# Optimization experiments

Hardware: AMD Instinct MI355X
Metric: run time of the kernel (lower is better)

## Reference

```python
import jax, jax.numpy as jnp
import numpy as np

BS, N, C_IMG, C_PT, H, W = 8, 100000, 512, 256, 48, 160


def setup_inputs() -> dict:
    key = jax.random.key(0)
    ks = jax.random.split(key, 8)
    point_feat = jax.random.normal(ks[0], (N, C_PT), dtype=jnp.float32)
    # pillar centers in LiDAR frame: x forward [10,60], y left [-10,10], z [-2,1]
    u = jax.random.uniform(ks[1], (N, 3), dtype=jnp.float32)
    pillar_centers = jnp.stack([
        10.0 + 50.0 * u[:, 0],
        -10.0 + 20.0 * u[:, 1],
        -2.0 + 3.0 * u[:, 2],
    ], axis=1)
    batch_idx = jax.random.randint(ks[2], (N,), 0, BS, dtype=jnp.int32)
    img_feat = jax.random.normal(ks[3], (BS, C_IMG, H, W), dtype=jnp.float32)
    # KITTI-style calibration (per batch, small jitter)
    f, cx, cy = 80.0, 80.0, 24.0
    P2_base = np.array([[f, 0, cx, 0], [0, f, cy, 0], [0, 0, 1, 0]], dtype=np.float32)
    Tr_base = np.array([[0, -1, 0, 0], [0, 0, -1, 0], [1, 0, 0, 0], [0, 0, 0, 1]], dtype=np.float32)
    rng = np.random.RandomState(0)
    P2 = np.stack([P2_base + 0.01 * rng.randn(3, 4).astype(np.float32) for _ in range(BS)])
    R0 = np.stack([np.eye(4, dtype=np.float32) for _ in range(BS)])
    Tr = np.stack([Tr_base + 0.001 * rng.randn(4, 4).astype(np.float32) for _ in range(BS)])
    align_w = jax.random.normal(ks[4], (C_PT, C_IMG), dtype=jnp.float32) * 0.02
    align_b = jax.random.normal(ks[5], (C_PT,), dtype=jnp.float32) * 0.02
    return {
        'point_feat': point_feat, 'pillar_centers': pillar_centers,
        'img_feat': img_feat, 'P2': jnp.asarray(P2), 'R0': jnp.asarray(R0),
        'Tr': jnp.asarray(Tr), 'align_w': align_w, 'align_b': align_b,
        'batch_idx': batch_idx, 'img_h': H, 'img_w': W,
    }


def _fuse(point_feat, pillar_centers, img_feat, P2, R0, Tr, align_w, align_b,
          batch_idx, img_h, img_w):
    n = point_feat.shape[0]
    dt = point_feat.dtype
    # --- project_to_image (vectorized over all points via per-point calib gather) ---
    pts_hom = jnp.concatenate([pillar_centers, jnp.ones((n, 1), dtype=dt)], axis=1)  # [N,4]
    pts_cam = jnp.einsum('nij,nj->ni', Tr[batch_idx], pts_hom)    # [N,4]
    pts_rect = jnp.einsum('nij,nj->ni', R0[batch_idx], pts_cam)   # [N,4]
    pts_img = jnp.einsum('nij,nj->ni', P2[batch_idx], pts_rect)   # [N,3]
    depth = jnp.clip(pts_img[:, 2:3], 1e-5, None)
    uv = pts_img[:, :2] / depth
    valid = ((pts_img[:, 2] > 0) & (uv[:, 0] >= 0) & (uv[:, 0] < img_w)
             & (uv[:, 1] >= 0) & (uv[:, 1] < img_h))
    # --- grid_sample bilinear, align_corners=True, padding_mode='zeros' ---
    # grid = 2*uv/(dim-1)-1 with align_corners=True => pixel coords == uv.
    _, C, Hf, Wf = img_feat.shape
    u_, v_ = uv[:, 0], uv[:, 1]
    x0 = jnp.floor(u_); y0 = jnp.floor(v_)
    wx1 = u_ - x0; wx0 = 1.0 - wx1
    wy1 = v_ - y0; wy0 = 1.0 - wy1

    def gather(xi, yi):
        inb = (xi >= 0) & (xi <= Wf - 1) & (yi >= 0) & (yi <= Hf - 1)
        xc = jnp.clip(xi, 0, Wf - 1).astype(jnp.int32)
        yc = jnp.clip(yi, 0, Hf - 1).astype(jnp.int32)
        f = img_feat[batch_idx, :, yc, xc]  # [N,C]
        return f * inb.astype(dt)[:, None]

    sampled = (gather(x0, y0) * (wx0 * wy0)[:, None]
               + gather(x0 + 1, y0) * (wx1 * wy0)[:, None]
               + gather(x0, y0 + 1) * (wx0 * wy1)[:, None]
               + gather(x0 + 1, y0 + 1) * (wx1 * wy1)[:, None])
    sampled = jnp.where(valid[:, None], sampled, jnp.zeros((), dtype=dt))
    # --- align (Linear) + residual add ---
    aligned = sampled @ align_w.T + align_b
    return point_feat + aligned


def reference(point_feat, pillar_centers, img_feat, P2, R0, Tr, align_w, align_b,
              batch_idx, img_h, img_w):
    return _fuse(point_feat, pillar_centers, img_feat, P2, R0, Tr,
                 align_w, align_b, batch_idx, img_h, img_w)
```

## Files before the change

### kernel.cpp

```cpp
#include <hip/hip_runtime.h>

#define C_IMG 512
#define C_PT  256
#define IMG_H 48
#define IMG_W 160
#define HWPIX (IMG_H * IMG_W)

#define MP   64
#define BK   64
#define SPAD 72

typedef short bf16x8 __attribute__((ext_vector_type(8)));
typedef float f32x4  __attribute__((ext_vector_type(4)));

static __device__ __forceinline__ unsigned short f2bf(float f) {
    unsigned u = __float_as_uint(f);
    u += 0x7fffu + ((u >> 16) & 1u);
    return (unsigned short)(u >> 16);
}
static __device__ __forceinline__ unsigned pack2(float lo, float hi) {
    return (unsigned)f2bf(lo) | ((unsigned)f2bf(hi) << 16);
}
static __device__ __forceinline__ float bflo(unsigned v) { return __uint_as_float(v << 16); }
static __device__ __forceinline__ float bfhi(unsigned v) { return __uint_as_float(v & 0xffff0000u); }

__global__ __launch_bounds__(256)
void cvt_w_kernel(const float* __restrict__ alw, unsigned short* __restrict__ alwT) {
    const int i = (blockIdx.x * 256 + threadIdx.x) * 8;
    const float4 a = *(const float4*)(alw + i);
    const float4 b = *(const float4*)(alw + i + 4);
    uint4 o;
    o.x = pack2(a.x, a.y); o.y = pack2(a.z, a.w);
    o.z = pack2(b.x, b.y); o.w = pack2(b.z, b.w);
    *(uint4*)(alwT + i) = o;
}

__global__ __launch_bounds__(256)
void proj_kernel(const float* __restrict__ img,
                 const unsigned short* __restrict__ wbf,
                 unsigned short* __restrict__ PT) {
    const int blk  = blockIdx.x;
    const int b    = blk / (HWPIX / 64);
    const int hw0  = (blk % (HWPIX / 64)) * 64;
    const int tid  = threadIdx.x;
    const int lane = tid & 63;
    const int wid  = tid >> 6;
    const int l15  = lane & 15;
    const int quad = lane >> 4;

    f32x4 acc[4][4];
    #pragma unroll
    for (int i = 0; i < 4; ++i)
        #pragma unroll
        for (int j = 0; j < 4; ++j)
            acc[i][j] = (f32x4){0.f, 0.f, 0.f, 0.f};

    const float* aim = img + (size_t)b * C_IMG * HWPIX + hw0 + l15;
    const unsigned short* bw = wbf + (size_t)(wid * 64 + l15) * C_IMG + quad * 8;

    for (int ck = 0; ck < C_IMG / 64; ++ck) {
        #pragma unroll
        for (int kk = 0; kk < 2; ++kk) {
            const int c0 = ck * 64 + kk * 32 + quad * 8;
            bf16x8 af[4];
            #pragma unroll
            for (int mt = 0; mt < 4; ++mt) {
                const float* ap = aim + (size_t)c0 * HWPIX + mt * 16;
                float f[8];
                #pragma unroll
                for (int j = 0; j < 8; ++j) f[j] = ap[j * HWPIX];
                union { unsigned u[4]; bf16x8 v; } cv;
                cv.u[0] = pack2(f[0], f[1]);
                cv.u[1] = pack2(f[2], f[3]);
                cv.u[2] = pack2(f[4], f[5]);
                cv.u[3] = pack2(f[6], f[7]);
                af[mt] = cv.v;
            }
            bf16x8 bfr[4];
            #pragma unroll
            for (int nt = 0; nt < 4; ++nt)
                bfr[nt] = *(const bf16x8*)(bw + (size_t)(nt * 16) * C_IMG + ck * 64 + kk * 32);
            #pragma unroll
            for (int mt = 0; mt < 4; ++mt)
                #pragma unroll
                for (int nt = 0; nt < 4; ++nt)
                    acc[mt][nt] = __builtin_amdgcn_mfma_f32_16x16x32_bf16(
                        af[mt], bfr[nt], acc[mt][nt], 0, 0, 0);
        }
    }

    #pragma unroll
    for (int mt = 0; mt < 4; ++mt) {
        #pragma unroll
        for (int r = 0; r < 4; ++r) {
            const int pix = mt * 16 + quad * 4 + r;
            unsigned short* dst = PT + (size_t)(b * HWPIX + hw0 + pix) * C_PT;
            #pragma unroll
            for (int nt = 0; nt < 4; ++nt) {
                const int nc = wid * 64 + nt * 16 + l15;
                dst[nc] = f2bf(acc[mt][nt][r]);
            }
        }
    }
}

#define PPW 4
__global__ __launch_bounds__(256)
void point_kernel(const float* __restrict__ pf,
                  const float* __restrict__ centers,
                  const unsigned short* __restrict__ PT,
                  const float* __restrict__ P2,
                  const float* __restrict__ R0,
                  const float* __restrict__ Tr,
                  const float* __restrict__ alb,
                  const int*   __restrict__ bidx,
                  float* __restrict__ out,
                  int n)
{
    const int tid  = threadIdx.x;
    const int lane = tid & 63;
    const int wid  = tid >> 6;
    const int p0   = blockIdx.x * (4 * PPW) + wid * PPW;

    const float4 ab = *(const float4*)(alb + lane * 4);

    #pragma unroll
    for (int it = 0; it < PPW; ++it) {
        const int p = p0 + it;
        if (p >= n) break;

        const float cx = centers[p * 3 + 0];
        const float cy = centers[p * 3 + 1];
        const float cz = centers[p * 3 + 2];
        const int   b  = bidx[p];
        const float* tr = Tr + b * 16;
        const float c0 = tr[0]*cx + tr[1]*cy + tr[2]*cz + tr[3];
        const float c1 = tr[4]*cx + tr[5]*cy + tr[6]*cz + tr[7];
        const float c2 = tr[8]*cx + tr[9]*cy + tr[10]*cz + tr[11];
        const float c3 = tr[12]*cx + tr[13]*cy + tr[14]*cz + tr[15];
        const float* r0 = R0 + b * 16;
        const float e0 = r0[0]*c0 + r0[1]*c1 + r0[2]*c2 + r0[3]*c3;
        const float e1 = r0[4]*c0 + r0[5]*c1 + r0[6]*c2 + r0[7]*c3;
        const float e2 = r0[8]*c0 + r0[9]*c1 + r0[10]*c2 + r0[11]*c3;
        const float e3 = r0[12]*c0 + r0[13]*c1 + r0[14]*c2 + r0[15]*c3;
        const float* p2 = P2 + b * 12;
        const float ix = p2[0]*e0 + p2[1]*e1 + p2[2]*e2  + p2[3]*e3;
        const float iy = p2[4]*e0 + p2[5]*e1 + p2[6]*e2  + p2[7]*e3;
        const float iz = p2[8]*e0 + p2[9]*e1 + p2[10]*e2 + p2[11]*e3;
        const float depth = fmaxf(iz, 1e-5f);
        const float u = ix / depth;
        const float v = iy / depth;
        const bool valid = (iz > 0.f) && (u >= 0.f) && (u < (float)IMG_W)
                                     && (v >= 0.f) && (v < (float)IMG_H);
        const float x0f = floorf(u), y0f = floorf(v);
        const float wx1 = u - x0f, wx0 = 1.f - wx1;
        const float wy1 = v - y0f, wy0 = 1.f - wy1;
        const float cwv[4] = {wx0 * wy0, wx1 * wy0, wx0 * wy1, wx1 * wy1};
        float wgt[4]; int off[4];
        #pragma unroll
        for (int j = 0; j < 4; ++j) {
            const float xf = x0f + (float)(j & 1);
            const float yf = y0f + (float)(j >> 1);
            const bool inb = (xf >= 0.f) && (xf <= (float)(IMG_W - 1))
                          && (yf >= 0.f) && (yf <= (float)(IMG_H - 1));
            const int xc = (int)fminf(fmaxf(xf, 0.f), (float)(IMG_W - 1));
            const int yc = (int)fminf(fmaxf(yf, 0.f), (float)(IMG_H - 1));
            wgt[j] = (valid && inb) ? cwv[j] : 0.f;
            off[j] = ((b * IMG_H + yc) * IMG_W + xc) * C_PT;
        }

        float s0 = 0.f, s1 = 0.f, s2 = 0.f, s3 = 0.f;
        #pragma unroll
        for (int j = 0; j < 4; ++j) {
            const uint2 g = *(const uint2*)(PT + off[j] + lane * 4);
            s0 = fmaf(wgt[j], bflo(g.x), s0);
            s1 = fmaf(wgt[j], bfhi(g.x), s1);
            s2 = fmaf(wgt[j], bflo(g.y), s2);
            s3 = fmaf(wgt[j], bfhi(g.y), s3);
        }

        const size_t idx = (size_t)p * C_PT + lane * 4;
        const float4 pv = *(const float4*)(pf + idx);
        float4 ov;
        ov.x = pv.x + ab.x + s0;
        ov.y = pv.y + ab.y + s1;
        ov.z = pv.z + ab.z + s2;
        ov.w = pv.w + ab.w + s3;
        *(float4*)(out + idx) = ov;
    }
}

__global__ __launch_bounds__(256)
void fused_fallback_kernel(const float* __restrict__ pf,
                           const float* __restrict__ centers,
                           const float* __restrict__ img,
                           const float* __restrict__ P2,
                           const float* __restrict__ R0,
                           const float* __restrict__ Tr,
                           const float* __restrict__ alw,
                           const float* __restrict__ alb,
                           const int*   __restrict__ bidx,
                           float* __restrict__ out,
                           int n)
{
    __shared__ float          sWg[MP][4];
    __shared__ int            sOf[MP][4];
    __shared__ unsigned short sS[MP][SPAD];
    __shared__ unsigned short sW[C_PT][SPAD];

    const int tid = threadIdx.x;
    const int pt0 = blockIdx.x * MP;

    if (tid < MP) {
        const int p = pt0 + tid;
        float w[4] = {0.f, 0.f, 0.f, 0.f};
        int   o[4] = {0, 0, 0, 0};
        if (p < n) {
            const float cx = centers[p * 3 + 0];
            const float cy = centers[p * 3 + 1];
            const float cz = centers[p * 3 + 2];
            const int   b  = bidx[p];
            const float* tr = Tr + b * 16;
            const float c0 = tr[0]*cx + tr[1]*cy + tr[2]*cz + tr[3];
            const float c1 = tr[4]*cx + tr[5]*cy + tr[6]*cz + tr[7];
            const float c2 = tr[8]*cx + tr[9]*cy + tr[10]*cz + tr[11];
            const float c3 = tr[12]*cx + tr[13]*cy + tr[14]*cz + tr[15];
            const float* r0 = R0 + b * 16;
            const float e0 = r0[0]*c0 + r0[1]*c1 + r0[2]*c2 + r0[3]*c3;
            const float e1 = r0[4]*c0 + r0[5]*c1 + r0[6]*c2 + r0[7]*c3;
            const float e2 = r0[8]*c0 + r0[9]*c1 + r0[10]*c2 + r0[11]*c3;
            const float e3 = r0[12]*c0 + r0[13]*c1 + r0[14]*c2 + r0[15]*c3;
            const float* p2 = P2 + b * 12;
            const float ix = p2[0]*e0 + p2[1]*e1 + p2[2]*e2  + p2[3]*e3;
            const float iy = p2[4]*e0 + p2[5]*e1 + p2[6]*e2  + p2[7]*e3;
            const float iz = p2[8]*e0 + p2[9]*e1 + p2[10]*e2 + p2[11]*e3;
            const float depth = fmaxf(iz, 1e-5f);
            const float u = ix / depth;
            const float v = iy / depth;
            const bool valid = (iz > 0.f) && (u >= 0.f) && (u < (float)IMG_W)
                                         && (v >= 0.f) && (v < (float)IMG_H);
            const float x0f = floorf(u), y0f = floorf(v);
            const float wx1 = u - x0f, wx0 = 1.f - wx1;
            const float wy1 = v - y0f, wy0 = 1.f - wy1;
            const float cwv[4] = {wx0 * wy0, wx1 * wy0, wx0 * wy1, wx1 * wy1};
            #pragma unroll
            for (int j = 0; j < 4; ++j) {
                const float xf = x0f + (float)(j & 1);
                const float yf = y0f + (float)(j >> 1);
                const bool inb = (xf >= 0.f) && (xf <= (float)(IMG_W - 1))
                              && (yf >= 0.f) && (yf <= (float)(IMG_H - 1));
                const int xc = (int)fminf(fmaxf(xf, 0.f), (float)(IMG_W - 1));
                const int yc = (int)fminf(fmaxf(yf, 0.f), (float)(IMG_H - 1));
                w[j] = (valid && inb) ? cwv[j] : 0.f;
                o[j] = b * C_IMG * HWPIX + yc * IMG_W + xc;
            }
        }
        #pragma unroll
        for (int j = 0; j < 4; ++j) { sWg[tid][j] = w[j]; sOf[tid][j] = o[j]; }
    }

    f32x4 acc[4][4];
    #pragma unroll
    for (int i = 0; i < 4; ++i)
        #pragma unroll
        for (int j = 0; j < 4; ++j)
            acc[i][j] = (f32x4){0.f, 0.f, 0.f, 0.f};

    const int lane = tid & 63;
    const int wid  = tid >> 6;
    const int l15  = lane & 15;
    const int quad = lane >> 4;
    const int sp   = tid >> 2;
    const int ssub = tid & 3;

    __syncthreads();

    for (int ck = 0; ck < C_IMG / BK; ++ck) {
        {
            const float cw0 = sWg[sp][0], cw1 = sWg[sp][1], cw2 = sWg[sp][2], cw3 = sWg[sp][3];
            const int   co0 = sOf[sp][0], co1 = sOf[sp][1], co2 = sOf[sp][2], co3 = sOf[sp][3];
            const int   cb  = ck * BK + ssub * 16;
            const float* ib = img;
            #pragma unroll
            for (int h = 0; h < 2; ++h) {
                uint4 ov;
                unsigned* op = (unsigned*)&ov;
                #pragma unroll
                for (int wI = 0; wI < 4; ++wI) {
                    const int c = cb + h * 8 + 2 * wI;
                    const float vlo = cw0*ib[co0 + c*HWPIX] + cw1*ib[co1 + c*HWPIX]
                                    + cw2*ib[co2 + c*HWPIX] + cw3*ib[co3 + c*HWPIX];
                    const float vhi = cw0*ib[co0 + (c+1)*HWPIX] + cw1*ib[co1 + (c+1)*HWPIX]
                                    + cw2*ib[co2 + (c+1)*HWPIX] + cw3*ib[co3 + (c+1)*HWPIX];
                    op[wI] = pack2(vlo, vhi);
                }
                *(uint4*)&sS[sp][ssub * 16 + h * 8] = ov;
            }
        }
        {
            #pragma unroll
            for (int pass = 0; pass < 4; ++pass) {
                const int r = pass * 64 + (tid >> 2);
                const int c = (tid & 3) * 16;
                const float* wr = alw + (size_t)r * C_IMG + ck * BK + c;
                const float4 f0 = *(const float4*)(wr + 0);
                const float4 f1 = *(const float4*)(wr + 4);
                const float4 f2 = *(const float4*)(wr + 8);
                const float4 f3 = *(const float4*)(wr + 12);
                uint4 oa, ob;
                oa.x = pack2(f0.x, f0.y); oa.y = pack2(f0.z, f0.w);
                oa.z = pack2(f1.x, f1.y); oa.w = pack2(f1.z, f1.w);
                ob.x = pack2(f2.x, f2.y); ob.y = pack2(f2.z, f2.w);
                ob.z = pack2(f3.x, f3.y); ob.w = pack2(f3.z, f3.w);
                *(uint4*)&sW[r][c]     = oa;
                *(uint4*)&sW[r][c + 8] = ob;
            }
        }
        __syncthreads();

        #pragma unroll
        for (int kk = 0; kk < 2; ++kk) {
            bf16x8 af[4], bfr[4];
            #pragma unroll
            for (int mt = 0; mt < 4; ++mt)
                af[mt] = *(const bf16x8*)&sS[mt * 16 + l15][kk * 32 + quad * 8];
            #pragma unroll
            for (int nt = 0; nt < 4; ++nt)
                bfr[nt] = *(const bf16x8*)&sW[wid * 64 + nt * 16 + l15][kk * 32 + quad * 8];
            #pragma unroll
            for (int mt = 0; mt < 4; ++mt)
                #pragma unroll
                for (int nt = 0; nt < 4; ++nt)
                    acc[mt][nt] = __builtin_amdgcn_mfma_f32_16x16x32_bf16(
                        af[mt], bfr[nt], acc[mt][nt], 0, 0, 0);
        }
        __syncthreads();
    }

    #pragma unroll
    for (int mt = 0; mt < 4; ++mt) {
        #pragma unroll
        for (int r = 0; r < 4; ++r) {
            const int p = pt0 + mt * 16 + quad * 4 + r;
            if (p < n) {
                #pragma unroll
                for (int nt = 0; nt < 4; ++nt) {
                    const int nc = wid * 64 + nt * 16 + l15;
                    const size_t idx = (size_t)p * C_PT + nc;
                    out[idx] = pf[idx] + alb[nc] + acc[mt][nt][r];
                }
            }
        }
    }
}

extern "C" void kernel_launch(void* const* d_in, const int* in_sizes, int n_in,
                              void* d_out, int out_size, void* d_ws, size_t ws_size,
                              hipStream_t stream) {
    const float* pf      = (const float*)d_in[0];
    const float* centers = (const float*)d_in[1];
    const float* img     = (const float*)d_in[2];
    const float* P2      = (const float*)d_in[3];
    const float* R0      = (const float*)d_in[4];
    const float* Tr      = (const float*)d_in[5];
    const float* alw     = (const float*)d_in[6];
    const float* alb     = (const float*)d_in[7];
    const int*   bidx    = (const int*)d_in[8];
    float*       out     = (float*)d_out;

    const int n  = in_sizes[8];
    const int bs = in_sizes[3] / 12;

    const size_t tpt = (size_t)bs * HWPIX * C_PT * sizeof(unsigned short);
    const size_t tw  = (size_t)C_PT * C_IMG * sizeof(unsigned short);
    if (ws_size >= tpt + tw) {
        unsigned short* PT  = (unsigned short*)d_ws;
        unsigned short* wbf = (unsigned short*)((char*)d_ws + tpt);
        cvt_w_kernel<<<(C_PT * C_IMG / 8) / 256, 256, 0, stream>>>(alw, wbf);
        proj_kernel<<<bs * (HWPIX / 64), 256, 0, stream>>>(img, wbf, PT);
        point_kernel<<<(n + 4 * PPW * 4 - 1) / (4 * PPW * 4) * 4, 256, 0, stream>>>(
            pf, centers, PT, P2, R0, Tr, alb, bidx, out, n);
    } else {
        const int nblk = (n + MP - 1) / MP;
        fused_fallback_kernel<<<nblk, 256, 0, stream>>>(
            pf, centers, img, P2, R0, Tr, alw, alb, bidx, out, n);
    }
}
```

Before: 386.5 us.

## Stage image tiles in LDS, precompute point params, widen point gathers

The projection GEMM now loads the fp32 image channels through a double-buffered, swizzled LDS tile with coalesced float4 loads, replacing strided scalar global loads. It also uses cheaper round-half-up bf16 conversion. A new params kernel computes each point's bilinear offsets and weights once, and the point kernel reads them and gathers 8 channels per lane with nontemporal loads and stores on the dense point features. The cost is an extra kernel launch, extra workspace traffic, and slightly different bf16 rounding.

```diff
diff --git a/kernel.cpp b/kernel.cpp
--- a/kernel.cpp
+++ b/kernel.cpp
@@ -12,6 +12,7 @@
 
 typedef short bf16x8 __attribute__((ext_vector_type(8)));
 typedef float f32x4  __attribute__((ext_vector_type(4)));
+typedef unsigned u32x4 __attribute__((ext_vector_type(4)));
 
 static __device__ __forceinline__ unsigned short f2bf(float f) {
     unsigned u = __float_as_uint(f);
@@ -20,6 +21,13 @@
 }
 static __device__ __forceinline__ unsigned pack2(float lo, float hi) {
     return (unsigned)f2bf(lo) | ((unsigned)f2bf(hi) << 16);
+}
+static __device__ __forceinline__ unsigned short f2bf_hu(float f) {
+    return (unsigned short)((__float_as_uint(f) + 0x8000u) >> 16);
+}
+static __device__ __forceinline__ unsigned pack2_hu(float lo, float hi) {
+    return ((__float_as_uint(lo) + 0x8000u) >> 16)
+         | ((__float_as_uint(hi) + 0x8000u) & 0xffff0000u);
 }
 static __device__ __forceinline__ float bflo(unsigned v) { return __uint_as_float(v << 16); }
 static __device__ __forceinline__ float bfhi(unsigned v) { return __uint_as_float(v & 0xffff0000u); }
@@ -36,9 +44,66 @@
 }
 
 __global__ __launch_bounds__(256)
+void params_kernel(const float* __restrict__ centers,
+                   const float* __restrict__ P2,
+                   const float* __restrict__ R0,
+                   const float* __restrict__ Tr,
+                   const int*   __restrict__ bidx,
+                   u32x4* __restrict__ poff,
+                   f32x4* __restrict__ pwgt,
+                   int n)
+{
+    const int p = blockIdx.x * 256 + threadIdx.x;
+    if (p >= n) return;
+    const float cx = centers[p * 3 + 0];
+    const float cy = centers[p * 3 + 1];
+    const float cz = centers[p * 3 + 2];
+    const int   b  = bidx[p];
+    const float* tr = Tr + b * 16;
+    const float c0 = tr[0]*cx + tr[1]*cy + tr[2]*cz + tr[3];
+    const float c1 = tr[4]*cx + tr[5]*cy + tr[6]*cz + tr[7];
+    const float c2 = tr[8]*cx + tr[9]*cy + tr[10]*cz + tr[11];
+    const float c3 = tr[12]*cx + tr[13]*cy + tr[14]*cz + tr[15];
+    const float* r0 = R0 + b * 16;
+    const float e0 = r0[0]*c0 + r0[1]*c1 + r0[2]*c2 + r0[3]*c3;
+    const float e1 = r0[4]*c0 + r0[5]*c1 + r0[6]*c2 + r0[7]*c3;
+    const float e2 = r0[8]*c0 + r0[9]*c1 + r0[10]*c2 + r0[11]*c3;
+    const float e3 = r0[12]*c0 + r0[13]*c1 + r0[14]*c2 + r0[15]*c3;
+    const float* p2 = P2 + b * 12;
+    const float ix = p2[0]*e0 + p2[1]*e1 + p2[2]*e2  + p2[3]*e3;
+    const float iy = p2[4]*e0 + p2[5]*e1 + p2[6]*e2  + p2[7]*e3;
+    const float iz = p2[8]*e0 + p2[9]*e1 + p2[10]*e2 + p2[11]*e3;
+    const float depth = fmaxf(iz, 1e-5f);
+    const float u = ix / depth;
+    const float v = iy / depth;
+    const bool valid = (iz > 0.f) && (u >= 0.f) && (u < (float)IMG_W)
+                                 && (v >= 0.f) && (v < (float)IMG_H);
+    const float x0f = floorf(u), y0f = floorf(v);
+    const float wx1 = u - x0f, wx0 = 1.f - wx1;
+    const float wy1 = v - y0f, wy0 = 1.f - wy1;
+    const float cwv[4] = {wx0 * wy0, wx1 * wy0, wx0 * wy1, wx1 * wy1};
+    f32x4 wg; u32x4 of;
+    #pragma unroll
+    for (int j = 0; j < 4; ++j) {
+        const float xf = x0f + (float)(j & 1);
+        const float yf = y0f + (float)(j >> 1);
+        const bool inb = (xf >= 0.f) && (xf <= (float)(IMG_W - 1))
+                      && (yf >= 0.f) && (yf <= (float)(IMG_H - 1));
+        const int xc = (int)fminf(fmaxf(xf, 0.f), (float)(IMG_W - 1));
+        const int yc = (int)fminf(fmaxf(yf, 0.f), (float)(IMG_H - 1));
+        wg[j] = (valid && inb) ? cwv[j] : 0.f;
+        of[j] = (unsigned)(((b * IMG_H + yc) * IMG_W + xc) * C_PT);
+    }
+    poff[p] = of;
+    pwgt[p] = wg;
+}
+
+__global__ __launch_bounds__(256)
 void proj_kernel(const float* __restrict__ img,
                  const unsigned short* __restrict__ wbf,
-                 unsigned short* __restrict__ PT) {
+                 unsigned short* __restrict__ PT)
+{
+    __shared__ float sF[2][64][68];
     const int blk  = blockIdx.x;
     const int b    = blk / (HWPIX / 64);
     const int hw0  = (blk % (HWPIX / 64)) * 64;
@@ -48,6 +113,11 @@
     const int l15  = lane & 15;
     const int quad = lane >> 4;
 
+    const int sr   = tid >> 2;
+    const int scc  = tid & 3;
+    const int sdst = ((scc ^ ((sr >> 3) & 3)) << 4);
+    const float* gsrc = img + (size_t)b * C_IMG * HWPIX + hw0 + scc * 16;
+
     f32x4 acc[4][4];
     #pragma unroll
     for (int i = 0; i < 4; ++i)
@@ -55,31 +125,44 @@
         for (int j = 0; j < 4; ++j)
             acc[i][j] = (f32x4){0.f, 0.f, 0.f, 0.f};
 
-    const float* aim = img + (size_t)b * C_IMG * HWPIX + hw0 + l15;
     const unsigned short* bw = wbf + (size_t)(wid * 64 + l15) * C_IMG + quad * 8;
 
+    float4 st[4];
+    {
+        const float* gp = gsrc + (size_t)sr * HWPIX;
+        #pragma unroll
+        for (int k = 0; k < 4; ++k) st[k] = *(const float4*)(gp + 4 * k);
+        #pragma unroll
+        for (int k = 0; k < 4; ++k) *(float4*)&sF[0][sr][sdst + 4 * k] = st[k];
+    }
+    __syncthreads();
+
     for (int ck = 0; ck < C_IMG / 64; ++ck) {
+        const int cur = ck & 1;
+        if (ck < C_IMG / 64 - 1) {
+            const float* gp = gsrc + (size_t)((ck + 1) * 64 + sr) * HWPIX;
+            #pragma unroll
+            for (int k = 0; k < 4; ++k) st[k] = *(const float4*)(gp + 4 * k);
+        }
         #pragma unroll
         for (int kk = 0; kk < 2; ++kk) {
-            const int c0 = ck * 64 + kk * 32 + quad * 8;
-            bf16x8 af[4];
-            #pragma unroll
-            for (int mt = 0; mt < 4; ++mt) {
-                const float* ap = aim + (size_t)c0 * HWPIX + mt * 16;
-                float f[8];
-                #pragma unroll
-                for (int j = 0; j < 8; ++j) f[j] = ap[j * HWPIX];
-                union { unsigned u[4]; bf16x8 v; } cv;
-                cv.u[0] = pack2(f[0], f[1]);
-                cv.u[1] = pack2(f[2], f[3]);
-                cv.u[2] = pack2(f[4], f[5]);
-                cv.u[3] = pack2(f[6], f[7]);
-                af[mt] = cv.v;
-            }
-            bf16x8 bfr[4];
+            bf16x8 af[4], bfr[4];
             #pragma unroll
             for (int nt = 0; nt < 4; ++nt)
                 bfr[nt] = *(const bf16x8*)(bw + (size_t)(nt * 16) * C_IMG + ck * 64 + kk * 32);
+            const int rbase = kk * 32 + quad * 8;
+            #pragma unroll
+            for (int mt = 0; mt < 4; ++mt) {
+                const int col = ((mt ^ quad) << 4) + l15;
+                float f[8];
+                #pragma unroll
+                for (int j = 0; j < 8; ++j) f[j] = sF[cur][rbase + j][col];
+                union { unsigned u[4]; bf16x8 v; } cv;
+                #pragma unroll
+                for (int w2 = 0; w2 < 4; ++w2)
+                    cv.u[w2] = pack2_hu(f[2 * w2], f[2 * w2 + 1]);
+                af[mt] = cv.v;
+            }
             #pragma unroll
             for (int mt = 0; mt < 4; ++mt)
                 #pragma unroll
@@ -87,6 +170,11 @@
                     acc[mt][nt] = __builtin_amdgcn_mfma_f32_16x16x32_bf16(
                         af[mt], bfr[nt], acc[mt][nt], 0, 0, 0);
         }
+        if (ck < C_IMG / 64 - 1) {
+            #pragma unroll
+            for (int k = 0; k < 4; ++k) *(float4*)&sF[cur ^ 1][sr][sdst + 4 * k] = st[k];
+        }
+        __syncthreads();
     }
 
     #pragma unroll
@@ -94,99 +182,61 @@
         #pragma unroll
         for (int r = 0; r < 4; ++r) {
             const int pix = mt * 16 + quad * 4 + r;
-            unsigned short* dst = PT + (size_t)(b * HWPIX + hw0 + pix) * C_PT;
-            #pragma unroll
-            for (int nt = 0; nt < 4; ++nt) {
-                const int nc = wid * 64 + nt * 16 + l15;
-                dst[nc] = f2bf(acc[mt][nt][r]);
-            }
-        }
-    }
-}
-
-#define PPW 4
+            unsigned short* dst = PT + (size_t)(b * HWPIX + hw0 + pix) * C_PT + wid * 64 + l15;
+            #pragma unroll
+            for (int nt = 0; nt < 4; ++nt)
+                dst[nt * 16] = f2bf_hu(acc[mt][nt][r]);
+        }
+    }
+}
+
 __global__ __launch_bounds__(256)
 void point_kernel(const float* __restrict__ pf,
-                  const float* __restrict__ centers,
                   const unsigned short* __restrict__ PT,
-                  const float* __restrict__ P2,
-                  const float* __restrict__ R0,
-                  const float* __restrict__ Tr,
                   const float* __restrict__ alb,
-                  const int*   __restrict__ bidx,
+                  const u32x4* __restrict__ poff,
+                  const f32x4* __restrict__ pwgt,
                   float* __restrict__ out,
                   int n)
 {
     const int tid  = threadIdx.x;
     const int lane = tid & 63;
     const int wid  = tid >> 6;
-    const int p0   = blockIdx.x * (4 * PPW) + wid * PPW;
-
-    const float4 ab = *(const float4*)(alb + lane * 4);
-
-    #pragma unroll
-    for (int it = 0; it < PPW; ++it) {
-        const int p = p0 + it;
-        if (p >= n) break;
-
-        const float cx = centers[p * 3 + 0];
-        const float cy = centers[p * 3 + 1];
-        const float cz = centers[p * 3 + 2];
-        const int   b  = bidx[p];
-        const float* tr = Tr + b * 16;
-        const float c0 = tr[0]*cx + tr[1]*cy + tr[2]*cz + tr[3];
-        const float c1 = tr[4]*cx + tr[5]*cy + tr[6]*cz + tr[7];
-        const float c2 = tr[8]*cx + tr[9]*cy + tr[10]*cz + tr[11];
-        const float c3 = tr[12]*cx + tr[13]*cy + tr[14]*cz + tr[15];
-        const float* r0 = R0 + b * 16;
-        const float e0 = r0[0]*c0 + r0[1]*c1 + r0[2]*c2 + r0[3]*c3;
-        const float e1 = r0[4]*c0 + r0[5]*c1 + r0[6]*c2 + r0[7]*c3;
-        const float e2 = r0[8]*c0 + r0[9]*c1 + r0[10]*c2 + r0[11]*c3;
-        const float e3 = r0[12]*c0 + r0[13]*c1 + r0[14]*c2 + r0[15]*c3;
-        const float* p2 = P2 + b * 12;
-        const float ix = p2[0]*e0 + p2[1]*e1 + p2[2]*e2  + p2[3]*e3;
-        const float iy = p2[4]*e0 + p2[5]*e1 + p2[6]*e2  + p2[7]*e3;
-        const float iz = p2[8]*e0 + p2[9]*e1 + p2[10]*e2 + p2[11]*e3;
-        const float depth = fmaxf(iz, 1e-5f);
-        const float u = ix / depth;
-        const float v = iy / depth;
-        const bool valid = (iz > 0.f) && (u >= 0.f) && (u < (float)IMG_W)
-                                     && (v >= 0.f) && (v < (float)IMG_H);
-        const float x0f = floorf(u), y0f = floorf(v);
-        const float wx1 = u - x0f, wx0 = 1.f - wx1;
-        const float wy1 = v - y0f, wy0 = 1.f - wy1;
-        const float cwv[4] = {wx0 * wy0, wx1 * wy0, wx0 * wy1, wx1 * wy1};
-        float wgt[4]; int off[4];
-        #pragma unroll
-        for (int j = 0; j < 4; ++j) {
-            const float xf = x0f + (float)(j & 1);
-            const float yf = y0f + (float)(j >> 1);
-            const bool inb = (xf >= 0.f) && (xf <= (float)(IMG_W - 1))
-                          && (yf >= 0.f) && (yf <= (float)(IMG_H - 1));
-            const int xc = (int)fminf(fmaxf(xf, 0.f), (float)(IMG_W - 1));
-            const int yc = (int)fminf(fmaxf(yf, 0.f), (float)(IMG_H - 1));
-            wgt[j] = (valid && inb) ? cwv[j] : 0.f;
-            off[j] = ((b * IMG_H + yc) * IMG_W + xc) * C_PT;
-        }
-
-        float s0 = 0.f, s1 = 0.f, s2 = 0.f, s3 = 0.f;
-        #pragma unroll
-        for (int j = 0; j < 4; ++j) {
-            const uint2 g = *(const uint2*)(PT + off[j] + lane * 4);
-            s0 = fmaf(wgt[j], bflo(g.x), s0);
-            s1 = fmaf(wgt[j], bfhi(g.x), s1);
-            s2 = fmaf(wgt[j], bflo(g.y), s2);
-            s3 = fmaf(wgt[j], bfhi(g.y), s3);
-        }
-
-        const size_t idx = (size_t)p * C_PT + lane * 4;
-        const float4 pv = *(const float4*)(pf + idx);
-        float4 ov;
-        ov.x = pv.x + ab.x + s0;
-        ov.y = pv.y + ab.y + s1;
-        ov.z = pv.z + ab.z + s2;
-        ov.w = pv.w + ab.w + s3;
-        *(float4*)(out + idx) = ov;
+    const int sub  = lane >> 5;
+    const int ch0  = (lane & 31) * 8;
+    const int base = blockIdx.x * 32 + wid * 8 + sub;
+
+    const f32x4 ab0 = *(const f32x4*)(alb + ch0);
+    const f32x4 ab1 = *(const f32x4*)(alb + ch0 + 4);
+
+    #pragma unroll
+    for (int it = 0; it < 4; ++it) {
+        const int p = base + it * 2;
+        if (p < n) {
+            const u32x4 of = poff[p];
+            const f32x4 wg = pwgt[p];
+            float s0 = 0.f, s1 = 0.f, s2 = 0.f, s3 = 0.f;
+            float s4 = 0.f, s5 = 0.f, s6 = 0.f, s7 = 0.f;
+            #pragma unroll
+            for (int j = 0; j < 4; ++j) {
+                const u32x4 g = *(const u32x4*)(PT + of[j] + ch0);
+                const float w = wg[j];
+                s0 = fmaf(w, bflo(g[0]), s0); s1 = fmaf(w, bfhi(g[0]), s1);
+                s2 = fmaf(w, bflo(g[1]), s2); s3 = fmaf(w, bfhi(g[1]), s3);
+                s4 = fmaf(w, bflo(g[2]), s4); s5 = fmaf(w, bfhi(g[2]), s5);
+                s6 = fmaf(w, bflo(g[3]), s6); s7 = fmaf(w, bfhi(g[3]), s7);
+            }
+            const size_t idx = (size_t)p * C_PT + ch0;
+            const f32x4 a  = __builtin_nontemporal_load((const f32x4*)(pf + idx));
+            const f32x4 b4 = __builtin_nontemporal_load((const f32x4*)(pf + idx + 4));
+            f32x4 o0, o1;
+            o0[0] = a[0] + ab0[0] + s0;  o0[1] = a[1] + ab0[1] + s1;
+            o0[2] = a[2] + ab0[2] + s2;  o0[3] = a[3] + ab0[3] + s3;
+            o1[0] = b4[0] + ab1[0] + s4; o1[1] = b4[1] + ab1[1] + s5;
+            o1[2] = b4[2] + ab1[2] + s6; o1[3] = b4[3] + ab1[3] + s7;
+            __builtin_nontemporal_store(o0, (f32x4*)(out + idx));
+            __builtin_nontemporal_store(o1, (f32x4*)(out + idx + 4));
+        }
     }
 }
 
@@ -373,13 +423,20 @@
 
     const size_t tpt = (size_t)bs * HWPIX * C_PT * sizeof(unsigned short);
     const size_t tw  = (size_t)C_PT * C_IMG * sizeof(unsigned short);
-    if (ws_size >= tpt + tw) {
+    const size_t tof = (size_t)n * 16;
+    const size_t twg = (size_t)n * 16;
+    if (ws_size >= tpt + tw + tof + twg) {
         unsigned short* PT  = (unsigned short*)d_ws;
         unsigned short* wbf = (unsigned short*)((char*)d_ws + tpt);
+        u32x4*          poff = (u32x4*)((char*)d_ws + tpt + tw);
+        f32x4*          pwgt = (f32x4*)((char*)d_ws + tpt + tw + tof);
+
         cvt_w_kernel<<<(C_PT * C_IMG / 8) / 256, 256, 0, stream>>>(alw, wbf);
+        params_kernel<<<(n + 255) / 256, 256, 0, stream>>>(
+            centers, P2, R0, Tr, bidx, poff, pwgt, n);
         proj_kernel<<<bs * (HWPIX / 64), 256, 0, stream>>>(img, wbf, PT);
-        point_kernel<<<(n + 4 * PPW * 4 - 1) / (4 * PPW * 4) * 4, 256, 0, stream>>>(
-            pf, centers, PT, P2, R0, Tr, alb, bidx, out, n);
+        point_kernel<<<(n + 31) / 32, 256, 0, stream>>>(
+            pf, PT, alb, poff, pwgt, out, n);
     } else {
         const int nblk = (n + MP - 1) / MP;
         fused_fallback_kernel<<<nblk, 256, 0, stream>>>(
```

New measurement: 334.8 us. -13.4%, faster.
